# Kernel tuning notes

Hardware: AMD Instinct MI355X
Metric: run time of the kernel (lower is better)

Reference implementation:

```python
import jax, jax.numpy as jnp
import numpy as np

B, L, D_INNER, D_STATE, DT_RANK = 1, 1024, 5120, 16, 160


def setup_inputs() -> dict:
    key = jax.random.key(0)
    k0, k1, k2, k3, k4, k5 = jax.random.split(key, 6)
    x = jax.random.normal(k0, (B, L, D_INNER), dtype=jnp.float32)
    # A_log in [0,1) -> A = -exp(A_log) in [-e,-1]: stable decaying recurrence
    A_log = jax.random.uniform(k1, (D_INNER, D_STATE), dtype=jnp.float32)
    D = jax.random.normal(k2, (D_INNER,), dtype=jnp.float32)
    x_proj_w = jax.random.normal(k3, (DT_RANK + 2 * D_STATE, D_INNER), dtype=jnp.float32) * 0.02
    dt_proj_w = jax.random.normal(k4, (D_INNER, DT_RANK), dtype=jnp.float32) * 0.02
    dt_proj_b = jax.random.normal(k5, (D_INNER,), dtype=jnp.float32) * 0.02
    return {"x": x, "A_log": A_log, "D": D, "x_proj_w": x_proj_w,
            "dt_proj_w": dt_proj_w, "dt_proj_b": dt_proj_b}


def reference(x, A_log, D, x_proj_w, dt_proj_w, dt_proj_b):
    # Mamba ssm(): x (b, l, d_inner) -> y (b, l, d_inner)
    A = -jnp.exp(A_log)                                   # (d, n)
    x_dbl = jnp.einsum('bld,ed->ble', x, x_proj_w)        # (b, l, dt_rank+2n)
    dt = x_dbl[..., :DT_RANK]                             # (b, l, r)
    Bm = x_dbl[..., DT_RANK:DT_RANK + D_STATE]            # (b, l, n)
    Cm = x_dbl[..., DT_RANK + D_STATE:]                   # (b, l, n)
    delta = jax.nn.softplus(jnp.einsum('blr,dr->bld', dt, dt_proj_w) + dt_proj_b)

    # discretization (zero-order hold)
    deltaA = jnp.exp(jnp.einsum('bld,dn->bldn', delta, A))        # (b, l, d, n)
    deltaB_u = jnp.einsum('bld,bln,bld->bldn', delta, Bm, x)      # (b, l, d, n)

    def step(h, inp):
        dA_t, dBu_t, c_t = inp          # (b,d,n), (b,d,n), (b,n)
        h = dA_t * h + dBu_t
        y_t = jnp.einsum('bdn,bn->bd', h, c_t)
        return h, y_t

    h0 = jnp.zeros((x.shape[0], D_INNER, D_STATE), dtype=x.dtype)
    xs = (jnp.swapaxes(deltaA, 0, 1),   # (l, b, d, n)
          jnp.swapaxes(deltaB_u, 0, 1),
          jnp.swapaxes(Cm, 0, 1))
    _, ys = jax.lax.scan(step, h0, xs)  # ys: (l, b, d)
    y = jnp.swapaxes(ys, 0, 1)          # (b, l, d)
    return y + x * D
```

## Files before the change

### kernel.cpp

```cpp
#include <hip/hip_runtime.h>
#include <hip/hip_bf16.h>

#define L_SEQ 1024
#define DI    5120
#define DS    16
#define DR    160
#define NE    192
#define NC    16
#define CL    64
#define SPLITK 16
#define KSPLIT (DI / SPLITK)
#define BK    64
#define LOG2E 1.44269504088896340736f

#define OFF_P     0
#define OFF_XDBL  12582912
#define OFF_WH    13369344
#define OFF_WL    15007744
#define OFF_XH    16646144
#define OFF_XL    17039360
#define OFF_XPH   17432576
#define OFF_XPL   27918336
#define OFF_XWH   38404096
#define OFF_XWL   40370176
#define OFF_ZB    42336256
#define OFF_HEND  84279296
#define OFF_APROD 89522176

typedef short s16x8 __attribute__((ext_vector_type(8)));
typedef float f32x4 __attribute__((ext_vector_type(4)));

__device__ __forceinline__ unsigned short bf_rn(float f) {
  unsigned u = __float_as_uint(f);
  u += 0x7FFFu + ((u >> 16) & 1u);
  return (unsigned short)(u >> 16);
}
__device__ __forceinline__ void split_hilo(float f, unsigned short& h, unsigned short& l) {
  h = bf_rn(f);
  float hf = __uint_as_float(((unsigned)h) << 16);
  l = bf_rn(f - hf);
}

__global__ __launch_bounds__(256) void k_cvt(const float* __restrict__ src,
                                             unsigned short* __restrict__ hi,
                                             unsigned short* __restrict__ lo,
                                             int n4) {
  int i = blockIdx.x * 256 + threadIdx.x;
  if (i >= n4) return;
  int i4 = i * 4;
  float4 v = *(const float4*)&src[i4];
  float f[4] = {v.x, v.y, v.z, v.w};
  ushort4 h, l;
  unsigned short hh, ll;
  split_hilo(f[0], hh, ll); h.x = hh; l.x = ll;
  split_hilo(f[1], hh, ll); h.y = hh; l.y = ll;
  split_hilo(f[2], hh, ll); h.z = hh; l.z = ll;
  split_hilo(f[3], hh, ll); h.w = hh; l.w = ll;
  *(ushort4*)&hi[i4] = h;
  *(ushort4*)&lo[i4] = l;
}

#define AST2 72
__global__ __launch_bounds__(256) void k_xdbl_mfma2(const unsigned short* __restrict__ xph,
                                                    const unsigned short* __restrict__ xpl,
                                                    const unsigned short* __restrict__ wxh,
                                                    const unsigned short* __restrict__ wxl,
                                                    float* __restrict__ part) {
  __shared__ unsigned short sAh[64 * AST2];
  __shared__ unsigned short sAl[64 * AST2];
  const int tid  = threadIdx.x;
  const int lane = tid & 63;
  const int w    = tid >> 6;
  const int wl_  = w >> 1;
  const int we   = w & 1;
  const int l0   = blockIdx.y * 64;
  const int e0   = blockIdx.x * 64 + we * 32;
  const int kb   = blockIdx.z * KSPLIT;
  const int rc   = lane & 15;
  const int kg   = (lane >> 4) * 8;

  f32x4 acc[2][2] = {};
  for (int k0 = 0; k0 < KSPLIT; k0 += BK) {
    __syncthreads();
    for (int idx = tid; idx < 64 * 8; idx += 256) {
      int r = idx >> 3, c8 = (idx & 7) * 8;
      *(s16x8*)&sAh[r * AST2 + c8] = *(const s16x8*)&xph[(size_t)(l0 + r) * DI + kb + k0 + c8];
      *(s16x8*)&sAl[r * AST2 + c8] = *(const s16x8*)&xpl[(size_t)(l0 + r) * DI + kb + k0 + c8];
    }
    __syncthreads();
#pragma unroll
    for (int ks = 0; ks < BK; ks += 32) {
      s16x8 ah[2], al[2], bh[2], bl[2];
#pragma unroll
      for (int mf = 0; mf < 2; ++mf) {
        int row = wl_ * 32 + mf * 16 + rc;
        ah[mf] = *(const s16x8*)&sAh[row * AST2 + ks + kg];
        al[mf] = *(const s16x8*)&sAl[row * AST2 + ks + kg];
      }
#pragma unroll
      for (int nf = 0; nf < 2; ++nf) {
        size_t e = e0 + nf * 16 + rc;
        bh[nf] = *(const s16x8*)&wxh[e * DI + kb + k0 + ks + kg];
        bl[nf] = *(const s16x8*)&wxl[e * DI + kb + k0 + ks + kg];
      }
#pragma unroll
      for (int mf = 0; mf < 2; ++mf)
#pragma unroll
        for (int nf = 0; nf < 2; ++nf) {
          acc[mf][nf] = __builtin_amdgcn_mfma_f32_16x16x32_bf16(ah[mf], bh[nf], acc[mf][nf], 0, 0, 0);
          acc[mf][nf] = __builtin_amdgcn_mfma_f32_16x16x32_bf16(ah[mf], bl[nf], acc[mf][nf], 0, 0, 0);
          acc[mf][nf] = __builtin_amdgcn_mfma_f32_16x16x32_bf16(al[mf], bh[nf], acc[mf][nf], 0, 0, 0);
        }
    }
  }
#pragma unroll
  for (int mf = 0; mf < 2; ++mf)
#pragma unroll
    for (int nf = 0; nf < 2; ++nf)
#pragma unroll
      for (int r = 0; r < 4; ++r) {
        int l = l0 + wl_ * 32 + mf * 16 + (lane >> 4) * 4 + r;
        int e = e0 + nf * 16 + rc;
        part[((size_t)blockIdx.z * L_SEQ + l) * NE + e] = acc[mf][nf][r];
      }
}

__global__ __launch_bounds__(256) void k_xdbl_reduce(const float* __restrict__ part,
                                                     float* __restrict__ xdbl,
                                                     unsigned short* __restrict__ xh,
                                                     unsigned short* __restrict__ xl) {
  int i4 = (blockIdx.x * 256 + threadIdx.x) * 4;
  float4 s = {0.f, 0.f, 0.f, 0.f};
#pragma unroll
  for (int z = 0; z < SPLITK; ++z) {
    float4 p = *(const float4*)&part[(size_t)z * L_SEQ * NE + i4];
    s.x += p.x; s.y += p.y; s.z += p.z; s.w += p.w;
  }
  *(float4*)&xdbl[i4] = s;
  float f[4] = {s.x, s.y, s.z, s.w};
  ushort4 h, l;
  unsigned short hh, ll;
  split_hilo(f[0], hh, ll); h.x = hh; l.x = ll;
  split_hilo(f[1], hh, ll); h.y = hh; l.y = ll;
  split_hilo(f[2], hh, ll); h.z = hh; l.z = ll;
  split_hilo(f[3], hh, ll); h.w = hh; l.w = ll;
  *(ushort4*)&xh[i4] = h;
  *(ushort4*)&xl[i4] = l;
}

#define AST 168
#define DST 129
__global__ __launch_bounds__(512) void k_delta_scan1(const unsigned short* __restrict__ xh,
                                                     const unsigned short* __restrict__ xl,
                                                     const unsigned short* __restrict__ wh,
                                                     const unsigned short* __restrict__ wlo,
                                                     const float* __restrict__ dtb,
                                                     const float* __restrict__ x,
                                                     const float* __restrict__ xdbl,
                                                     const float* __restrict__ A_log,
                                                     float2* __restrict__ zbuf,
                                                     float* __restrict__ hend,
                                                     float* __restrict__ aprod) {
  __shared__ __align__(16) unsigned char smem[64 * AST * 2 * 2];
  unsigned short* sAh = (unsigned short*)smem;
  unsigned short* sAl = sAh + 64 * AST;
  const int tid  = threadIdx.x;
  const int lane = tid & 63;
  const int w    = tid >> 6;
  const int wl_  = w >> 2;
  const int wd   = w & 3;
  const int c    = blockIdx.y;
  const int l0   = c * 64;
  const int d0b  = blockIdx.x * 128;
  const int d0   = d0b + wd * 32;
  const int rc   = lane & 15;
  const int kg   = (lane >> 4) * 8;

  for (int idx = tid; idx < 64 * 20; idx += 512) {
    int r = idx / 20, c8 = (idx % 20) * 8;
    *(s16x8*)&sAh[r * AST + c8] = *(const s16x8*)&xh[(size_t)(l0 + r) * NE + c8];
    *(s16x8*)&sAl[r * AST + c8] = *(const s16x8*)&xl[(size_t)(l0 + r) * NE + c8];
  }
  __syncthreads();

  f32x4 acc[2][2] = {};
#pragma unroll
  for (int k0 = 0; k0 < DR; k0 += 32) {
    s16x8 ah[2], al[2], bh[2], bl[2];
#pragma unroll
    for (int mf = 0; mf < 2; ++mf) {
      int row = wl_ * 32 + mf * 16 + rc;
      ah[mf] = *(const s16x8*)&sAh[row * AST + k0 + kg];
      al[mf] = *(const s16x8*)&sAl[row * AST + k0 + kg];
    }
#pragma unroll
    for (int nf = 0; nf < 2; ++nf) {
      size_t d = d0 + nf * 16 + rc;
      bh[nf] = *(const s16x8*)&wh[d * DR + k0 + kg];
      bl[nf] = *(const s16x8*)&wlo[d * DR + k0 + kg];
    }
#pragma unroll
    for (int mf = 0; mf < 2; ++mf)
#pragma unroll
      for (int nf = 0; nf < 2; ++nf) {
        acc[mf][nf] = __builtin_amdgcn_mfma_f32_16x16x32_bf16(ah[mf], bh[nf], acc[mf][nf], 0, 0, 0);
        acc[mf][nf] = __builtin_amdgcn_mfma_f32_16x16x32_bf16(ah[mf], bl[nf], acc[mf][nf], 0, 0, 0);
        acc[mf][nf] = __builtin_amdgcn_mfma_f32_16x16x32_bf16(al[mf], bh[nf], acc[mf][nf], 0, 0, 0);
      }
  }
  __syncthreads();

  float* sDelta = (float*)smem;
  float* sB     = (float*)(smem + 64 * DST * 4);
  for (int i = tid; i < 64 * 16; i += 512) {
    int t = i >> 4, n = i & 15;
    sB[i] = xdbl[(size_t)(l0 + t) * NE + DR + n];
  }
#pragma unroll
  for (int nf = 0; nf < 2; ++nf) {
    int d = d0 + nf * 16 + rc;
    int dloc = d - d0b;
    float bias = dtb[d];
#pragma unroll
    for (int mf = 0; mf < 2; ++mf)
#pragma unroll
      for (int r = 0; r < 4; ++r) {
        int lloc = wl_ * 32 + mf * 16 + (lane >> 4) * 4 + r;
        int l = l0 + lloc;
        float z = acc[mf][nf][r] + bias;
        float sp = fmaxf(z, 0.f) + __logf(1.f + __expf(-fabsf(z)));
        float xv = x[(size_t)l * DI + d];
        sDelta[lloc * DST + dloc] = sp;
        zbuf[(size_t)l * DI + d] = make_float2(sp, xv);
      }
  }
  __syncthreads();

  const int dloc = tid & 127;
  const int ng   = tid >> 7;
  const int d    = d0b + dloc;
  float4 av = *(const float4*)&A_log[(size_t)d * DS + ng * 4];
  float aL[4] = {-__expf(av.x) * LOG2E, -__expf(av.y) * LOG2E,
                 -__expf(av.z) * LOG2E, -__expf(av.w) * LOG2E};
  float h[4] = {0.f, 0.f, 0.f, 0.f};
  float sdl = 0.f;
  const float* xp = &x[(size_t)l0 * DI + d];
  float xb[4];
#pragma unroll
  for (int j = 0; j < 4; ++j) xb[j] = xp[(size_t)j * DI];
  for (int tt = 0; tt < CL; tt += 4) {
    bool pf = (tt + 4 < CL);
#pragma unroll
    for (int j = 0; j < 4; ++j) {
      float xv = xb[j];
      if (pf) xb[j] = xp[(size_t)(tt + 4 + j) * DI];
      float dl = sDelta[(tt + j) * DST + dloc];
      float du = dl * xv;
      sdl += dl;
      float4 b4 = *(const float4*)&sB[(tt + j) * 16 + ng * 4];
      float bb[4] = {b4.x, b4.y, b4.z, b4.w};
#pragma unroll
      for (int q = 0; q < 4; ++q) {
        float dA = exp2f(dl * aL[q]);
        h[q] = dA * h[q] + du * bb[q];
      }
    }
  }
#pragma unroll
  for (int q = 0; q < 4; ++q) {
    int n = ng * 4 + q;
    hend[(size_t)(c * DS + n) * DI + d] = h[q];
    aprod[(size_t)(c * DS + n) * DI + d] = exp2f(aL[q] * sdl);
  }
}

__global__ __launch_bounds__(256) void k_scan2(float* __restrict__ hend,
                                               const float* __restrict__ aprod) {
  int i = blockIdx.x * 256 + threadIdx.x;
  float ap[NC], hv[NC];
#pragma unroll
  for (int c = 0; c < NC; ++c) {
    size_t idx = (size_t)c * DS * DI + i;
    ap[c] = aprod[idx];
    hv[c] = hend[idx];
  }
  float carry = 0.f;
#pragma unroll
  for (int c = 0; c < NC; ++c) {
    size_t idx = (size_t)c * DS * DI + i;
    hend[idx] = carry;
    carry = ap[c] * carry + hv[c];
  }
}

__global__ __launch_bounds__(256) void k_scan3(const float2* __restrict__ zbuf,
                                               const float* __restrict__ xdbl,
                                               const float* __restrict__ A_log,
                                               const float* __restrict__ Dvec,
                                               const float* __restrict__ hstart,
                                               float* __restrict__ out) {
  const int lane = threadIdx.x & 63;
  const int w    = threadIdx.x >> 6;
  const int d    = blockIdx.x * 64 + w * 16 + (lane & 15);
  const int ng   = lane >> 4;
  const int c    = blockIdx.y;
  __shared__ __align__(16) float sB[CL][DS];
  __shared__ __align__(16) float sC[CL][DS];
  for (int i = threadIdx.x; i < CL * DS; i += 256) {
    int t = i >> 4, n = i & 15;
    sB[t][n] = xdbl[(size_t)(c * CL + t) * NE + DR + n];
    sC[t][n] = xdbl[(size_t)(c * CL + t) * NE + DR + DS + n];
  }
  __syncthreads();
  float4 av = *(const float4*)&A_log[(size_t)d * DS + ng * 4];
  float aL[4] = {-__expf(av.x) * LOG2E, -__expf(av.y) * LOG2E,
                 -__expf(av.z) * LOG2E, -__expf(av.w) * LOG2E};
  float h[4];
#pragma unroll
  for (int q = 0; q < 4; ++q)
    h[q] = hstart[(size_t)(c * DS + ng * 4 + q) * DI + d];
  const float Dv = Dvec[d];
  const float2* zp = &zbuf[(size_t)(c * CL) * DI + d];
  float* op = &out[(size_t)(c * CL) * DI + d];
  float2 zb[8];
#pragma unroll
  for (int j = 0; j < 8; ++j) zb[j] = zp[(size_t)j * DI];
  for (int tt = 0; tt < CL; tt += 8) {
#pragma unroll
    for (int j = 0; j < 8; ++j) {
      float dl = zb[j].x, xv = zb[j].y;
      int tn = tt + 8 + j;
      if (tn < CL) zb[j] = zp[(size_t)tn * DI];
      float du = dl * xv;
      float4 b4 = *(const float4*)&sB[tt + j][ng * 4];
      float4 c4 = *(const float4*)&sC[tt + j][ng * 4];
      float bb[4] = {b4.x, b4.y, b4.z, b4.w};
      float cc[4] = {c4.x, c4.y, c4.z, c4.w};
      float y = 0.f;
#pragma unroll
      for (int q = 0; q < 4; ++q) {
        float dA = exp2f(dl * aL[q]);
        h[q] = dA * h[q] + du * bb[q];
        y += h[q] * cc[q];
      }
      y += __shfl_xor(y, 16, 64);
      y += __shfl_xor(y, 32, 64);
      if (ng == 0) op[(size_t)(tt + j) * DI] = fmaf(xv, Dv, y);
    }
  }
}

extern "C" void kernel_launch(void* const* d_in, const int* in_sizes, int n_in,
                              void* d_out, int out_size, void* d_ws, size_t ws_size,
                              hipStream_t stream) {
  const float* x     = (const float*)d_in[0];
  const float* A_log = (const float*)d_in[1];
  const float* Dvec  = (const float*)d_in[2];
  const float* xw    = (const float*)d_in[3];
  const float* dtw   = (const float*)d_in[4];
  const float* dtb   = (const float*)d_in[5];
  float* out = (float*)d_out;

  char* ws = (char*)d_ws;
  float* part  = (float*)(ws + OFF_P);
  float* xdbl  = (float*)(ws + OFF_XDBL);
  float* hend  = (float*)(ws + OFF_HEND);
  float* aprod = (float*)(ws + OFF_APROD);
  unsigned short* wh  = (unsigned short*)(ws + OFF_WH);
  unsigned short* wl  = (unsigned short*)(ws + OFF_WL);
  unsigned short* xh  = (unsigned short*)(ws + OFF_XH);
  unsigned short* xl  = (unsigned short*)(ws + OFF_XL);
  unsigned short* xph = (unsigned short*)(ws + OFF_XPH);
  unsigned short* xpl = (unsigned short*)(ws + OFF_XPL);
  unsigned short* wxh = (unsigned short*)(ws + OFF_XWH);
  unsigned short* wxl = (unsigned short*)(ws + OFF_XWL);
  float2* zbuf = (float2*)(ws + OFF_ZB);

  k_cvt<<<5120, 256, 0, stream>>>(x, xph, xpl, L_SEQ * DI / 4);
  k_cvt<<<960, 256, 0, stream>>>(xw, wxh, wxl, NE * DI / 4);
  k_cvt<<<800, 256, 0, stream>>>(dtw, wh, wl, DI * DR / 4);
  k_xdbl_mfma2<<<dim3(3, 16, SPLITK), 256, 0, stream>>>(xph, xpl, wxh, wxl, part);
  k_xdbl_reduce<<<192, 256, 0, stream>>>(part, xdbl, xh, xl);
  k_delta_scan1<<<dim3(40, 16), 512, 0, stream>>>(xh, xl, wh, wl, dtb, x, xdbl,
                                                  A_log, zbuf, hend, aprod);
  k_scan2<<<320, 256, 0, stream>>>(hend, aprod);
  k_scan3<<<dim3(80, 16), 256, 0, stream>>>(zbuf, xdbl, A_log, Dvec, hend, out);
}
```

Before: 120.8 us.

## Split delta GEMM from chunk scan and stage zbuf tiles in LDS

Unfuses the delta projection and first chunk scan into two kernels. The new scan1 kernel reads delta and x back from zbuf, using 64-wide d blocks with a 4-way state split. Both scan kernels now load the whole chunk's zbuf tile into shared memory with coalesced loads before the recurrence, replacing strided per-thread global prefetch. This adds a kernel launch and an extra zbuf round trip, in exchange for better occupancy and latency hiding in the scans.

```diff
diff --git a/kernel.cpp b/kernel.cpp
--- a/kernel.cpp
+++ b/kernel.cpp
@@ -149,30 +149,22 @@
 }
 
 #define AST 168
-#define DST 129
-__global__ __launch_bounds__(512) void k_delta_scan1(const unsigned short* __restrict__ xh,
+__global__ __launch_bounds__(512) void k_delta_mfma2(const unsigned short* __restrict__ xh,
                                                      const unsigned short* __restrict__ xl,
                                                      const unsigned short* __restrict__ wh,
                                                      const unsigned short* __restrict__ wlo,
                                                      const float* __restrict__ dtb,
                                                      const float* __restrict__ x,
-                                                     const float* __restrict__ xdbl,
-                                                     const float* __restrict__ A_log,
-                                                     float2* __restrict__ zbuf,
-                                                     float* __restrict__ hend,
-                                                     float* __restrict__ aprod) {
-  __shared__ __align__(16) unsigned char smem[64 * AST * 2 * 2];
-  unsigned short* sAh = (unsigned short*)smem;
-  unsigned short* sAl = sAh + 64 * AST;
+                                                     float2* __restrict__ zbuf) {
+  __shared__ unsigned short sAh[64 * AST];
+  __shared__ unsigned short sAl[64 * AST];
   const int tid  = threadIdx.x;
   const int lane = tid & 63;
   const int w    = tid >> 6;
   const int wl_  = w >> 2;
   const int wd   = w & 3;
-  const int c    = blockIdx.y;
-  const int l0   = c * 64;
-  const int d0b  = blockIdx.x * 128;
-  const int d0   = d0b + wd * 32;
+  const int l0   = blockIdx.y * 64;
+  const int d0   = blockIdx.x * 128 + wd * 32;
   const int rc   = lane & 15;
   const int kg   = (lane >> 4) * 8;
 
@@ -208,62 +200,66 @@
         acc[mf][nf] = __builtin_amdgcn_mfma_f32_16x16x32_bf16(al[mf], bh[nf], acc[mf][nf], 0, 0, 0);
       }
   }
-  __syncthreads();
-
-  float* sDelta = (float*)smem;
-  float* sB     = (float*)(smem + 64 * DST * 4);
-  for (int i = tid; i < 64 * 16; i += 512) {
-    int t = i >> 4, n = i & 15;
-    sB[i] = xdbl[(size_t)(l0 + t) * NE + DR + n];
-  }
 #pragma unroll
   for (int nf = 0; nf < 2; ++nf) {
     int d = d0 + nf * 16 + rc;
-    int dloc = d - d0b;
     float bias = dtb[d];
 #pragma unroll
     for (int mf = 0; mf < 2; ++mf)
 #pragma unroll
       for (int r = 0; r < 4; ++r) {
-        int lloc = wl_ * 32 + mf * 16 + (lane >> 4) * 4 + r;
-        int l = l0 + lloc;
+        int l = l0 + wl_ * 32 + mf * 16 + (lane >> 4) * 4 + r;
         float z = acc[mf][nf][r] + bias;
         float sp = fmaxf(z, 0.f) + __logf(1.f + __expf(-fabsf(z)));
         float xv = x[(size_t)l * DI + d];
-        sDelta[lloc * DST + dloc] = sp;
         zbuf[(size_t)l * DI + d] = make_float2(sp, xv);
       }
   }
+}
+
+__global__ __launch_bounds__(256) void k_scan1L(const float2* __restrict__ zbuf,
+                                                const float* __restrict__ xdbl,
+                                                const float* __restrict__ A_log,
+                                                float* __restrict__ hend,
+                                                float* __restrict__ aprod) {
+  const int tid  = threadIdx.x;
+  const int lane = tid & 63;
+  const int w    = tid >> 6;
+  const int dloc = w * 16 + (lane & 15);
+  const int d    = blockIdx.x * 64 + dloc;
+  const int ng   = lane >> 4;
+  const int c    = blockIdx.y;
+  __shared__ __align__(16) float2 sZ[CL][65];
+  __shared__ __align__(16) float  sB[CL][DS];
+
+  const float2* zsrc = &zbuf[(size_t)(c * CL) * DI + blockIdx.x * 64];
+  for (int i = tid; i < CL * 64; i += 256) {
+    int t = i >> 6, dd = i & 63;
+    sZ[t][dd] = zsrc[(size_t)t * DI + dd];
+  }
+  for (int i = tid; i < CL * DS; i += 256) {
+    int t = i >> 4, n = i & 15;
+    sB[t][n] = xdbl[(size_t)(c * CL + t) * NE + DR + n];
+  }
   __syncthreads();
 
-  const int dloc = tid & 127;
-  const int ng   = tid >> 7;
-  const int d    = d0b + dloc;
   float4 av = *(const float4*)&A_log[(size_t)d * DS + ng * 4];
   float aL[4] = {-__expf(av.x) * LOG2E, -__expf(av.y) * LOG2E,
                  -__expf(av.z) * LOG2E, -__expf(av.w) * LOG2E};
   float h[4] = {0.f, 0.f, 0.f, 0.f};
   float sdl = 0.f;
-  const float* xp = &x[(size_t)l0 * DI + d];
-  float xb[4];
-#pragma unroll
-  for (int j = 0; j < 4; ++j) xb[j] = xp[(size_t)j * DI];
-  for (int tt = 0; tt < CL; tt += 4) {
-    bool pf = (tt + 4 < CL);
-#pragma unroll
-    for (int j = 0; j < 4; ++j) {
-      float xv = xb[j];
-      if (pf) xb[j] = xp[(size_t)(tt + 4 + j) * DI];
-      float dl = sDelta[(tt + j) * DST + dloc];
-      float du = dl * xv;
-      sdl += dl;
-      float4 b4 = *(const float4*)&sB[(tt + j) * 16 + ng * 4];
-      float bb[4] = {b4.x, b4.y, b4.z, b4.w};
-#pragma unroll
-      for (int q = 0; q < 4; ++q) {
-        float dA = exp2f(dl * aL[q]);
-        h[q] = dA * h[q] + du * bb[q];
-      }
+#pragma unroll 4
+  for (int t = 0; t < CL; ++t) {
+    float2 z = sZ[t][dloc];
+    float dl = z.x, xv = z.y;
+    float du = dl * xv;
+    sdl += dl;
+    float4 b4 = *(const float4*)&sB[t][ng * 4];
+    float bb[4] = {b4.x, b4.y, b4.z, b4.w};
+#pragma unroll
+    for (int q = 0; q < 4; ++q) {
+      float dA = exp2f(dl * aL[q]);
+      h[q] = dA * h[q] + du * bb[q];
     }
   }
 #pragma unroll
@@ -293,25 +289,35 @@
   }
 }
 
-__global__ __launch_bounds__(256) void k_scan3(const float2* __restrict__ zbuf,
-                                               const float* __restrict__ xdbl,
-                                               const float* __restrict__ A_log,
-                                               const float* __restrict__ Dvec,
-                                               const float* __restrict__ hstart,
-                                               float* __restrict__ out) {
-  const int lane = threadIdx.x & 63;
-  const int w    = threadIdx.x >> 6;
-  const int d    = blockIdx.x * 64 + w * 16 + (lane & 15);
+__global__ __launch_bounds__(256) void k_scan3L(const float2* __restrict__ zbuf,
+                                                const float* __restrict__ xdbl,
+                                                const float* __restrict__ A_log,
+                                                const float* __restrict__ Dvec,
+                                                const float* __restrict__ hstart,
+                                                float* __restrict__ out) {
+  const int tid  = threadIdx.x;
+  const int lane = tid & 63;
+  const int w    = tid >> 6;
+  const int dloc = w * 16 + (lane & 15);
+  const int d    = blockIdx.x * 64 + dloc;
   const int ng   = lane >> 4;
   const int c    = blockIdx.y;
-  __shared__ __align__(16) float sB[CL][DS];
-  __shared__ __align__(16) float sC[CL][DS];
-  for (int i = threadIdx.x; i < CL * DS; i += 256) {
+  __shared__ __align__(16) float2 sZ[CL][65];
+  __shared__ __align__(16) float  sB[CL][DS];
+  __shared__ __align__(16) float  sC[CL][DS];
+
+  const float2* zsrc = &zbuf[(size_t)(c * CL) * DI + blockIdx.x * 64];
+  for (int i = tid; i < CL * 64; i += 256) {
+    int t = i >> 6, dd = i & 63;
+    sZ[t][dd] = zsrc[(size_t)t * DI + dd];
+  }
+  for (int i = tid; i < CL * DS; i += 256) {
     int t = i >> 4, n = i & 15;
     sB[t][n] = xdbl[(size_t)(c * CL + t) * NE + DR + n];
     sC[t][n] = xdbl[(size_t)(c * CL + t) * NE + DR + DS + n];
   }
   __syncthreads();
+
   float4 av = *(const float4*)&A_log[(size_t)d * DS + ng * 4];
   float aL[4] = {-__expf(av.x) * LOG2E, -__expf(av.y) * LOG2E,
                  -__expf(av.z) * LOG2E, -__expf(av.w) * LOG2E};
@@ -320,33 +326,26 @@
   for (int q = 0; q < 4; ++q)
     h[q] = hstart[(size_t)(c * DS + ng * 4 + q) * DI + d];
   const float Dv = Dvec[d];
-  const float2* zp = &zbuf[(size_t)(c * CL) * DI + d];
   float* op = &out[(size_t)(c * CL) * DI + d];
-  float2 zb[8];
-#pragma unroll
-  for (int j = 0; j < 8; ++j) zb[j] = zp[(size_t)j * DI];
-  for (int tt = 0; tt < CL; tt += 8) {
-#pragma unroll
-    for (int j = 0; j < 8; ++j) {
-      float dl = zb[j].x, xv = zb[j].y;
-      int tn = tt + 8 + j;
-      if (tn < CL) zb[j] = zp[(size_t)tn * DI];
-      float du = dl * xv;
-      float4 b4 = *(const float4*)&sB[tt + j][ng * 4];
-      float4 c4 = *(const float4*)&sC[tt + j][ng * 4];
-      float bb[4] = {b4.x, b4.y, b4.z, b4.w};
-      float cc[4] = {c4.x, c4.y, c4.z, c4.w};
-      float y = 0.f;
-#pragma unroll
-      for (int q = 0; q < 4; ++q) {
-        float dA = exp2f(dl * aL[q]);
-        h[q] = dA * h[q] + du * bb[q];
-        y += h[q] * cc[q];
-      }
-      y += __shfl_xor(y, 16, 64);
-      y += __shfl_xor(y, 32, 64);
-      if (ng == 0) op[(size_t)(tt + j) * DI] = fmaf(xv, Dv, y);
-    }
+#pragma unroll 4
+  for (int t = 0; t < CL; ++t) {
+    float2 z = sZ[t][dloc];
+    float dl = z.x, xv = z.y;
+    float du = dl * xv;
+    float4 b4 = *(const float4*)&sB[t][ng * 4];
+    float4 c4 = *(const float4*)&sC[t][ng * 4];
+    float bb[4] = {b4.x, b4.y, b4.z, b4.w};
+    float cc[4] = {c4.x, c4.y, c4.z, c4.w};
+    float y = 0.f;
+#pragma unroll
+    for (int q = 0; q < 4; ++q) {
+      float dA = exp2f(dl * aL[q]);
+      h[q] = dA * h[q] + du * bb[q];
+      y += h[q] * cc[q];
+    }
+    y += __shfl_xor(y, 16, 64);
+    y += __shfl_xor(y, 32, 64);
+    if (ng == 0) op[(size_t)t * DI] = fmaf(xv, Dv, y);
   }
 }
 
@@ -381,8 +380,8 @@
   k_cvt<<<800, 256, 0, stream>>>(dtw, wh, wl, DI * DR / 4);
   k_xdbl_mfma2<<<dim3(3, 16, SPLITK), 256, 0, stream>>>(xph, xpl, wxh, wxl, part);
   k_xdbl_reduce<<<192, 256, 0, stream>>>(part, xdbl, xh, xl);
-  k_delta_scan1<<<dim3(40, 16), 512, 0, stream>>>(xh, xl, wh, wl, dtb, x, xdbl,
-                                                  A_log, zbuf, hend, aprod);
+  k_delta_mfma2<<<dim3(40, 16), 512, 0, stream>>>(xh, xl, wh, wl, dtb, x, zbuf);
+  k_scan1L<<<dim3(80, NC), 256, 0, stream>>>(zbuf, xdbl, A_log, hend, aprod);
   k_scan2<<<320, 256, 0, stream>>>(hend, aprod);
-  k_scan3<<<dim3(80, 16), 256, 0, stream>>>(zbuf, xdbl, A_log, Dvec, hend, out);
-}
+  k_scan3L<<<dim3(80, NC), 256, 0, stream>>>(zbuf, xdbl, A_log, Dvec, hend, out);
+}
```

Result: slower. 150.3 us (+24.4%).

## Split fused delta-GEMM/chunk-scan kernel into separate MFMA and scan kernels

Applied to the files above, without the earlier changes.

The fused kernel that computed delta via MFMA and then ran the first chunked scan pass in the same block is split into two kernels. The delta kernel now only writes (delta, x) pairs to zbuf. A new scan1 kernel reads zbuf from global memory with an 8-deep prefetch and uses a 4-waves-of-16-d layout like scan3. The split frees LDS and registers and gives the scan better occupancy and parallel layout, at the cost of an extra launch and a global re-read of zbuf.

```diff
diff --git a/kernel.cpp b/kernel.cpp
--- a/kernel.cpp
+++ b/kernel.cpp
@@ -149,30 +149,22 @@
 }
 
 #define AST 168
-#define DST 129
-__global__ __launch_bounds__(512) void k_delta_scan1(const unsigned short* __restrict__ xh,
+__global__ __launch_bounds__(512) void k_delta_mfma2(const unsigned short* __restrict__ xh,
                                                      const unsigned short* __restrict__ xl,
                                                      const unsigned short* __restrict__ wh,
                                                      const unsigned short* __restrict__ wlo,
                                                      const float* __restrict__ dtb,
                                                      const float* __restrict__ x,
-                                                     const float* __restrict__ xdbl,
-                                                     const float* __restrict__ A_log,
-                                                     float2* __restrict__ zbuf,
-                                                     float* __restrict__ hend,
-                                                     float* __restrict__ aprod) {
-  __shared__ __align__(16) unsigned char smem[64 * AST * 2 * 2];
-  unsigned short* sAh = (unsigned short*)smem;
-  unsigned short* sAl = sAh + 64 * AST;
+                                                     float2* __restrict__ zbuf) {
+  __shared__ unsigned short sAh[64 * AST];
+  __shared__ unsigned short sAl[64 * AST];
   const int tid  = threadIdx.x;
   const int lane = tid & 63;
   const int w    = tid >> 6;
   const int wl_  = w >> 2;
   const int wd   = w & 3;
-  const int c    = blockIdx.y;
-  const int l0   = c * 64;
-  const int d0b  = blockIdx.x * 128;
-  const int d0   = d0b + wd * 32;
+  const int l0   = blockIdx.y * 64;
+  const int d0   = blockIdx.x * 128 + wd * 32;
   const int rc   = lane & 15;
   const int kg   = (lane >> 4) * 8;
 
@@ -208,56 +200,57 @@
         acc[mf][nf] = __builtin_amdgcn_mfma_f32_16x16x32_bf16(al[mf], bh[nf], acc[mf][nf], 0, 0, 0);
       }
   }
-  __syncthreads();
-
-  float* sDelta = (float*)smem;
-  float* sB     = (float*)(smem + 64 * DST * 4);
-  for (int i = tid; i < 64 * 16; i += 512) {
-    int t = i >> 4, n = i & 15;
-    sB[i] = xdbl[(size_t)(l0 + t) * NE + DR + n];
-  }
 #pragma unroll
   for (int nf = 0; nf < 2; ++nf) {
     int d = d0 + nf * 16 + rc;
-    int dloc = d - d0b;
     float bias = dtb[d];
 #pragma unroll
     for (int mf = 0; mf < 2; ++mf)
 #pragma unroll
       for (int r = 0; r < 4; ++r) {
-        int lloc = wl_ * 32 + mf * 16 + (lane >> 4) * 4 + r;
-        int l = l0 + lloc;
+        int l = l0 + wl_ * 32 + mf * 16 + (lane >> 4) * 4 + r;
         float z = acc[mf][nf][r] + bias;
         float sp = fmaxf(z, 0.f) + __logf(1.f + __expf(-fabsf(z)));
         float xv = x[(size_t)l * DI + d];
-        sDelta[lloc * DST + dloc] = sp;
         zbuf[(size_t)l * DI + d] = make_float2(sp, xv);
       }
   }
+}
+
+__global__ __launch_bounds__(256) void k_scan1f(const float2* __restrict__ zbuf,
+                                                const float* __restrict__ xdbl,
+                                                const float* __restrict__ A_log,
+                                                float* __restrict__ hend,
+                                                float* __restrict__ aprod) {
+  const int lane = threadIdx.x & 63;
+  const int w    = threadIdx.x >> 6;
+  const int d    = blockIdx.x * 64 + w * 16 + (lane & 15);
+  const int ng   = lane >> 4;
+  const int c    = blockIdx.y;
+  __shared__ __align__(16) float sB[CL][DS];
+  for (int i = threadIdx.x; i < CL * DS; i += 256) {
+    int t = i >> 4, n = i & 15;
+    sB[t][n] = xdbl[(size_t)(c * CL + t) * NE + DR + n];
+  }
   __syncthreads();
-
-  const int dloc = tid & 127;
-  const int ng   = tid >> 7;
-  const int d    = d0b + dloc;
   float4 av = *(const float4*)&A_log[(size_t)d * DS + ng * 4];
   float aL[4] = {-__expf(av.x) * LOG2E, -__expf(av.y) * LOG2E,
                  -__expf(av.z) * LOG2E, -__expf(av.w) * LOG2E};
   float h[4] = {0.f, 0.f, 0.f, 0.f};
   float sdl = 0.f;
-  const float* xp = &x[(size_t)l0 * DI + d];
-  float xb[4];
-#pragma unroll
-  for (int j = 0; j < 4; ++j) xb[j] = xp[(size_t)j * DI];
-  for (int tt = 0; tt < CL; tt += 4) {
-    bool pf = (tt + 4 < CL);
-#pragma unroll
-    for (int j = 0; j < 4; ++j) {
-      float xv = xb[j];
-      if (pf) xb[j] = xp[(size_t)(tt + 4 + j) * DI];
-      float dl = sDelta[(tt + j) * DST + dloc];
+  const float2* zp = &zbuf[(size_t)(c * CL) * DI + d];
+  float2 zb[8];
+#pragma unroll
+  for (int j = 0; j < 8; ++j) zb[j] = zp[(size_t)j * DI];
+  for (int tt = 0; tt < CL; tt += 8) {
+#pragma unroll
+    for (int j = 0; j < 8; ++j) {
+      float dl = zb[j].x, xv = zb[j].y;
+      int tn = tt + 8 + j;
+      if (tn < CL) zb[j] = zp[(size_t)tn * DI];
       float du = dl * xv;
       sdl += dl;
-      float4 b4 = *(const float4*)&sB[(tt + j) * 16 + ng * 4];
+      float4 b4 = *(const float4*)&sB[tt + j][ng * 4];
       float bb[4] = {b4.x, b4.y, b4.z, b4.w};
 #pragma unroll
       for (int q = 0; q < 4; ++q) {
@@ -293,12 +286,12 @@
   }
 }
 
-__global__ __launch_bounds__(256) void k_scan3(const float2* __restrict__ zbuf,
-                                               const float* __restrict__ xdbl,
-                                               const float* __restrict__ A_log,
-                                               const float* __restrict__ Dvec,
-                                               const float* __restrict__ hstart,
-                                               float* __restrict__ out) {
+__global__ __launch_bounds__(256) void k_scan3f(const float2* __restrict__ zbuf,
+                                                const float* __restrict__ xdbl,
+                                                const float* __restrict__ A_log,
+                                                const float* __restrict__ Dvec,
+                                                const float* __restrict__ hstart,
+                                                float* __restrict__ out) {
   const int lane = threadIdx.x & 63;
   const int w    = threadIdx.x >> 6;
   const int d    = blockIdx.x * 64 + w * 16 + (lane & 15);
@@ -381,8 +374,8 @@
   k_cvt<<<800, 256, 0, stream>>>(dtw, wh, wl, DI * DR / 4);
   k_xdbl_mfma2<<<dim3(3, 16, SPLITK), 256, 0, stream>>>(xph, xpl, wxh, wxl, part);
   k_xdbl_reduce<<<192, 256, 0, stream>>>(part, xdbl, xh, xl);
-  k_delta_scan1<<<dim3(40, 16), 512, 0, stream>>>(xh, xl, wh, wl, dtb, x, xdbl,
-                                                  A_log, zbuf, hend, aprod);
+  k_delta_mfma2<<<dim3(40, 16), 512, 0, stream>>>(xh, xl, wh, wl, dtb, x, zbuf);
+  k_scan1f<<<dim3(80, NC), 256, 0, stream>>>(zbuf, xdbl, A_log, hend, aprod);
   k_scan2<<<320, 256, 0, stream>>>(hend, aprod);
-  k_scan3<<<dim3(80, 16), 256, 0, stream>>>(zbuf, xdbl, A_log, Dvec, hend, out);
-}
+  k_scan3f<<<dim3(80, NC), 256, 0, stream>>>(zbuf, xdbl, A_log, Dvec, hend, out);
+}
```

New measurement: 126.8 us. +5.0%, slower.
